# Performance work log

Measured on AMD Instinct MI355X. Metric: run time of the kernel, lower is better.

Reference implementation:

```python
import jax, jax.numpy as jnp
import numpy as np

B, LC, LQ, D = 16, 2048, 1024, 512


def setup_inputs() -> dict:
    key = jax.random.key(0)
    k1, k2, k3 = jax.random.split(key, 3)
    context = jax.random.normal(k1, (B, LC, D), dtype=jnp.float32)
    query = jax.random.normal(k2, (LQ, D), dtype=jnp.float32)
    # nn.Linear(3*D, 1, bias=False).weight  -> [1, 3D]
    w = jax.random.normal(k3, (1, 3 * D), dtype=jnp.float32) * (1.0 / np.sqrt(3 * D))
    return {"context": context, "query": query, "w": w}


def reference(context, query, w):
    # context: [B, Lc, D], query: [Lq, D], w: [1, 3D]
    d = context.shape[-1]
    wc, wq, wm = w[0, :d], w[0, d:2 * d], w[0, 2 * d:]
    # S[b,i,j] = <context[b,i], wc> + <query[j], wq> + <context[b,i]*wm, query[j]>
    # (algebraic collapse of Linear(cat(c, q, c*q)) -- identical math, no 4D tensor)
    S = ((context @ wc)[:, :, None]
         + (query @ wq)[None, None, :]
         + jnp.einsum('bid,jd->bij', context * wm, query))  # [B, Lc, Lq]
    # softmax over context dim (dim=1), then permute -> A[b,j,i]
    A = jnp.transpose(jax.nn.softmax(S, axis=1), (0, 2, 1))  # [B, Lq, Lc]
    # query mask: sign(|sum_d query|), same for every batch element
    qmask = jnp.sign(jnp.abs(jnp.sum(query, axis=-1)))  # [Lq]
    A = A * qmask[None, :, None]
    # attd[b,j,i,d] = A[b,j,i] * context[b,i,d]
    # G_att[b,i,d] = context[b,i,d] * sum_j A[b,j,i]
    colsum = jnp.sum(A, axis=1)  # [B, Lc]
    G_att = context * colsum[:, :, None]  # [B, Lc, D]
    # H[b,j,d] = sum_i A[b,j,i] * context[b,i,d]
    H = jnp.einsum('bji,bid->bjd', A, context)  # [B, Lq, D]
    G = jnp.concatenate((context, G_att), axis=2)  # [B, Lc, 2D]
    return (G, H)
```

## Files before the change

kernel.cpp:

```cpp
#include <hip/hip_runtime.h>
#include <stdint.h>

#define BB 16
#define LC 2048
#define LQ 1024
#define DD 512

typedef _Float16 f16x8 __attribute__((ext_vector_type(8)));
typedef _Float16 f16x4 __attribute__((ext_vector_type(4)));
typedef float f32x4 __attribute__((ext_vector_type(4)));

#define MFMA16 __builtin_amdgcn_mfma_f32_16x16x32_f16

__device__ __forceinline__ void async16(_Float16* lds, const _Float16* g) {
    __builtin_amdgcn_global_load_lds(
        (const __attribute__((address_space(1))) void*)g,
        (__attribute__((address_space(3))) void*)lds, 16, 0, 0);
}

__global__ void zero_k(float* __restrict__ p, int n) {
    int i = blockIdx.x * blockDim.x + threadIdx.x;
    if (i < n) p[i] = 0.0f;
}

__global__ __launch_bounds__(256) void prep_ctx(
    const float* __restrict__ ctx, const float* __restrict__ w,
    _Float16* __restrict__ cm, _Float16* __restrict__ ct, float* __restrict__ cb)
{
    __shared__ _Float16 sm[64][68];
    const int b = blockIdx.z;
    const int i0 = blockIdx.y * 64;
    const int d0 = blockIdx.x * 64;
    const int t = threadIdx.x;
    const int tx = t & 15, ty = t >> 4;
    const float* wc = w;
    const float* wm = w + 2 * DD;
    const float4 wc4 = *(const float4*)(wc + d0 + tx * 4);
    const float4 wm4 = *(const float4*)(wm + d0 + tx * 4);
    for (int k = 0; k < 4; ++k) {
        const int r = ty + 16 * k;
        const int ig = i0 + r;
        const float4 v = *(const float4*)(ctx + ((size_t)(b * LC + ig)) * DD + d0 + tx * 4);
        f16x4 cmv = { (_Float16)(v.x * wm4.x), (_Float16)(v.y * wm4.y),
                      (_Float16)(v.z * wm4.z), (_Float16)(v.w * wm4.w) };
        *(f16x4*)(cm + ((size_t)(b * LC + ig)) * DD + d0 + tx * 4) = cmv;
        sm[tx * 4 + 0][r] = (_Float16)v.x;
        sm[tx * 4 + 1][r] = (_Float16)v.y;
        sm[tx * 4 + 2][r] = (_Float16)v.z;
        sm[tx * 4 + 3][r] = (_Float16)v.w;
        float p = v.x * wc4.x + v.y * wc4.y + v.z * wc4.z + v.w * wc4.w;
        p += __shfl_xor(p, 1); p += __shfl_xor(p, 2);
        p += __shfl_xor(p, 4); p += __shfl_xor(p, 8);
        if (tx == 0) atomicAdd(&cb[b * LC + ig], p);
    }
    __syncthreads();
    for (int k = 0; k < 4; ++k) {
        const int dd = ty + 16 * k;
        f16x4 o = *(const f16x4*)(&sm[dd][tx * 4]);
        *(f16x4*)(ct + ((size_t)(b * DD + d0 + dd)) * LC + i0 + tx * 4) = o;
    }
}

__global__ __launch_bounds__(128) void prep_q(
    const float* __restrict__ q, const float* __restrict__ w,
    _Float16* __restrict__ qh, float* __restrict__ qb, float* __restrict__ qmask)
{
    const int j = blockIdx.x;
    const int t = threadIdx.x;
    const float* wq = w + DD;
    const float4 v = *(const float4*)(q + (size_t)j * DD + t * 4);
    const float4 wq4 = *(const float4*)(wq + t * 4);
    f16x4 qv = { (_Float16)v.x, (_Float16)v.y, (_Float16)v.z, (_Float16)v.w };
    *(f16x4*)(qh + (size_t)j * DD + t * 4) = qv;
    float dq = v.x * wq4.x + v.y * wq4.y + v.z * wq4.z + v.w * wq4.w;
    float sq = v.x + v.y + v.z + v.w;
    for (int m = 1; m < 64; m <<= 1) { dq += __shfl_xor(dq, m); sq += __shfl_xor(sq, m); }
    __shared__ float sd[2], ss[2];
    if ((t & 63) == 0) { sd[t >> 6] = dq; ss[t >> 6] = sq; }
    __syncthreads();
    if (t == 0) {
        qb[j] = sd[0] + sd[1];
        float s = ss[0] + ss[1];
        qmask[j] = (s != 0.0f) ? 1.0f : 0.0f;
    }
}

__global__ __launch_bounds__(256) void gemm1(
    const _Float16* __restrict__ qh, const _Float16* __restrict__ cm,
    const float* __restrict__ cb, const float* __restrict__ qb,
    _Float16* __restrict__ E, float* __restrict__ lsum)
{
    __shared__ __align__(16) _Float16 smA[128 * 32];
    __shared__ __align__(16) _Float16 smB[128 * 32];
    const int b = blockIdx.z;
    const int m0 = blockIdx.x * 128;
    const int n0 = blockIdx.y * 128;
    const int t = threadIdx.x;
    const int lane = t & 63;
    const int wid = t >> 6;
    const int wvm = wid >> 1, wvn = wid & 1;
    const int li = lane & 15, lg = lane >> 4;
    f32x4 acc[4][4] = {};
    const int srow = lane >> 2;
    const int scol = (lane & 3) * 8;
    const _Float16* gA0 = qh + (size_t)(m0 + wid * 32 + srow) * DD + scol;
    const _Float16* gA1 = gA0 + (size_t)16 * DD;
    const _Float16* gB0 = cm + ((size_t)(b * LC + n0 + wid * 32 + srow)) * DD + scol;
    const _Float16* gB1 = gB0 + (size_t)16 * DD;
    _Float16* sA0 = smA + wid * 32 * 32;
    _Float16* sA1 = sA0 + 16 * 32;
    _Float16* sB0 = smB + wid * 32 * 32;
    _Float16* sB1 = sB0 + 16 * 32;
    for (int ks = 0; ks < DD; ks += 32) {
        __syncthreads();
        async16(sA0, gA0 + ks);
        async16(sA1, gA1 + ks);
        async16(sB0, gB0 + ks);
        async16(sB1, gB1 + ks);
        __syncthreads();
        f16x8 af[4], bf[4];
        #pragma unroll
        for (int mt = 0; mt < 4; ++mt)
            af[mt] = *(const f16x8*)(smA + (wvm * 64 + mt * 16 + li) * 32 + lg * 8);
        #pragma unroll
        for (int nt = 0; nt < 4; ++nt)
            bf[nt] = *(const f16x8*)(smB + (wvn * 64 + nt * 16 + li) * 32 + lg * 8);
        #pragma unroll
        for (int mt = 0; mt < 4; ++mt)
            #pragma unroll
            for (int nt = 0; nt < 4; ++nt)
                acc[mt][nt] = MFMA16(af[mt], bf[nt], acc[mt][nt], 0, 0, 0);
    }
    __syncthreads();
    float* rs = (float*)smA;
    if (t < 128) rs[t] = 0.0f;
    __syncthreads();
    float cbv[4];
    #pragma unroll
    for (int nt = 0; nt < 4; ++nt) cbv[nt] = cb[b * LC + n0 + wvn * 64 + nt * 16 + li];
    #pragma unroll
    for (int mt = 0; mt < 4; ++mt) {
        #pragma unroll
        for (int r = 0; r < 4; ++r) {
            const int jl = wvm * 64 + mt * 16 + lg * 4 + r;
            const int j = m0 + jl;
            const float qbv = qb[j];
            _Float16* Erow = E + ((size_t)(b * LQ + j)) * LC + n0 + wvn * 64;
            float rsv = 0.0f;
            #pragma unroll
            for (int nt = 0; nt < 4; ++nt) {
                float e = __expf(acc[mt][nt][r] + cbv[nt] + qbv);
                rsv += e;
                Erow[nt * 16 + li] = (_Float16)e;
            }
            rsv += __shfl_xor(rsv, 1); rsv += __shfl_xor(rsv, 2);
            rsv += __shfl_xor(rsv, 4); rsv += __shfl_xor(rsv, 8);
            if (li == 0) atomicAdd(&rs[jl], rsv);
        }
    }
    __syncthreads();
    if (t < 128) atomicAdd(&lsum[b * LQ + m0 + t], rs[t]);
}

__global__ __launch_bounds__(256) void gemm2(
    const _Float16* __restrict__ E, const _Float16* __restrict__ ct,
    const float* __restrict__ lsum, const float* __restrict__ qmask,
    float* __restrict__ H)
{
    __shared__ __align__(16) _Float16 smA[128 * 32];
    __shared__ __align__(16) _Float16 smB[128 * 32];
    const int b = blockIdx.z;
    const int m0 = blockIdx.x * 128;
    const int n0 = blockIdx.y * 128;
    const int t = threadIdx.x;
    const int lane = t & 63;
    const int wid = t >> 6;
    const int wvm = wid >> 1, wvn = wid & 1;
    const int li = lane & 15, lg = lane >> 4;
    f32x4 acc[4][4] = {};
    const int srow = lane >> 2;
    const int scol = (lane & 3) * 8;
    const _Float16* gA0 = E + ((size_t)(b * LQ + m0 + wid * 32 + srow)) * LC + scol;
    const _Float16* gA1 = gA0 + (size_t)16 * LC;
    const _Float16* gB0 = ct + ((size_t)(b * DD + n0 + wid * 32 + srow)) * LC + scol;
    const _Float16* gB1 = gB0 + (size_t)16 * LC;
    _Float16* sA0 = smA + wid * 32 * 32;
    _Float16* sA1 = sA0 + 16 * 32;
    _Float16* sB0 = smB + wid * 32 * 32;
    _Float16* sB1 = sB0 + 16 * 32;
    for (int ks = 0; ks < LC; ks += 32) {
        __syncthreads();
        async16(sA0, gA0 + ks);
        async16(sA1, gA1 + ks);
        async16(sB0, gB0 + ks);
        async16(sB1, gB1 + ks);
        __syncthreads();
        f16x8 af[4], bf[4];
        #pragma unroll
        for (int mt = 0; mt < 4; ++mt)
            af[mt] = *(const f16x8*)(smA + (wvm * 64 + mt * 16 + li) * 32 + lg * 8);
        #pragma unroll
        for (int nt = 0; nt < 4; ++nt)
            bf[nt] = *(const f16x8*)(smB + (wvn * 64 + nt * 16 + li) * 32 + lg * 8);
        #pragma unroll
        for (int mt = 0; mt < 4; ++mt)
            #pragma unroll
            for (int nt = 0; nt < 4; ++nt)
                acc[mt][nt] = MFMA16(af[mt], bf[nt], acc[mt][nt], 0, 0, 0);
    }
    #pragma unroll
    for (int mt = 0; mt < 4; ++mt) {
        #pragma unroll
        for (int r = 0; r < 4; ++r) {
            const int j = m0 + wvm * 64 + mt * 16 + lg * 4 + r;
            const float s = qmask[j] / lsum[b * LQ + j];
            float* Hrow = H + ((size_t)(b * LQ + j)) * DD + n0 + wvn * 64;
            #pragma unroll
            for (int nt = 0; nt < 4; ++nt)
                Hrow[nt * 16 + li] = acc[mt][nt][r] * s;
        }
    }
}

__global__ __launch_bounds__(256) void colsum_k(
    const _Float16* __restrict__ E, const float* __restrict__ lsum,
    const float* __restrict__ qmask, float* __restrict__ cs)
{
    __shared__ float ssm[64];
    const int b = blockIdx.y;
    const int j0 = blockIdx.x * 64;
    const int t = threadIdx.x;
    if (t < 64) {
        const int jj = j0 + t;
        ssm[t] = qmask[jj] / lsum[b * LQ + jj];
    }
    __syncthreads();
    const _Float16* Eb = E + ((size_t)(b * LQ + j0)) * LC + t * 8;
    float acc[8] = {};
    #pragma unroll 4
    for (int j = 0; j < 64; ++j) {
        f16x8 v = *(const f16x8*)(Eb + (size_t)j * LC);
        const float s = ssm[j];
        #pragma unroll
        for (int q = 0; q < 8; ++q) acc[q] += s * (float)v[q];
    }
    float* base = cs + b * LC + t * 8;
    #pragma unroll
    for (int q = 0; q < 8; ++q) atomicAdd(base + q, acc[q]);
}

__global__ __launch_bounds__(128) void gwrite(
    const float* __restrict__ ctx, const float* __restrict__ cs, float* __restrict__ G)
{
    const int b = blockIdx.y, i = blockIdx.x, t = threadIdx.x;
    const float c = cs[b * LC + i];
    const size_t ro = (size_t)(b * LC + i);
    const float4 v = *(const float4*)(ctx + ro * DD + t * 4);
    float4 u; u.x = v.x * c; u.y = v.y * c; u.z = v.z * c; u.w = v.w * c;
    *(float4*)(G + ro * (2 * DD) + t * 4) = v;
    *(float4*)(G + ro * (2 * DD) + DD + t * 4) = u;
}

extern "C" void kernel_launch(void* const* d_in, const int* in_sizes, int n_in,
                              void* d_out, int out_size, void* d_ws, size_t ws_size,
                              hipStream_t stream)
{
    (void)in_sizes; (void)n_in; (void)out_size; (void)ws_size;
    const float* ctx = (const float*)d_in[0];
    const float* qry = (const float*)d_in[1];
    const float* w   = (const float*)d_in[2];
    float* G = (float*)d_out;
    float* H = G + (size_t)BB * LC * (2 * DD);

    char* ws = (char*)d_ws;
    _Float16* E  = (_Float16*)ws;
    _Float16* cm = (_Float16*)(ws + ((size_t)64 << 20));
    _Float16* ct = (_Float16*)(ws + ((size_t)96 << 20));
    _Float16* qh = (_Float16*)(ws + ((size_t)128 << 20));
    float* stats = (float*)(ws + ((size_t)130 << 20));
    float* cb    = stats;
    float* lsum  = cb + BB * LC;
    float* cs    = lsum + BB * LQ;
    float* qb    = cs + BB * LC;
    float* qmask = qb + LQ;

    const int nzero = BB * LC + BB * LQ + BB * LC;
    zero_k<<<dim3((nzero + 255) / 256), 256, 0, stream>>>(stats, nzero);
    prep_ctx<<<dim3(DD / 64, LC / 64, BB), 256, 0, stream>>>(ctx, w, cm, ct, cb);
    prep_q<<<dim3(LQ), 128, 0, stream>>>(qry, w, qh, qb, qmask);
    gemm1<<<dim3(LQ / 128, LC / 128, BB), 256, 0, stream>>>(qh, cm, cb, qb, E, lsum);
    gemm2<<<dim3(LQ / 128, DD / 128, BB), 256, 0, stream>>>(E, ct, lsum, qmask, H);
    colsum_k<<<dim3(LQ / 64, BB), 256, 0, stream>>>(E, lsum, qmask, cs);
    gwrite<<<dim3(LC, BB), 128, 0, stream>>>(ctx, cs, G);
}
```

Measured before the change: 390.9 us.

## Swap GEMM operand roles for vectorized epilogues, remap blocks, drop qb, atomic-free colsum

```diff
diff --git a/kernel.cpp b/kernel.cpp
--- a/kernel.cpp
+++ b/kernel.cpp
@@ -62,39 +62,33 @@
 }
 
 __global__ __launch_bounds__(128) void prep_q(
-    const float* __restrict__ q, const float* __restrict__ w,
-    _Float16* __restrict__ qh, float* __restrict__ qb, float* __restrict__ qmask)
+    const float* __restrict__ q, _Float16* __restrict__ qh, float* __restrict__ qmask)
 {
     const int j = blockIdx.x;
     const int t = threadIdx.x;
-    const float* wq = w + DD;
     const float4 v = *(const float4*)(q + (size_t)j * DD + t * 4);
-    const float4 wq4 = *(const float4*)(wq + t * 4);
     f16x4 qv = { (_Float16)v.x, (_Float16)v.y, (_Float16)v.z, (_Float16)v.w };
     *(f16x4*)(qh + (size_t)j * DD + t * 4) = qv;
-    float dq = v.x * wq4.x + v.y * wq4.y + v.z * wq4.z + v.w * wq4.w;
     float sq = v.x + v.y + v.z + v.w;
-    for (int m = 1; m < 64; m <<= 1) { dq += __shfl_xor(dq, m); sq += __shfl_xor(sq, m); }
-    __shared__ float sd[2], ss[2];
-    if ((t & 63) == 0) { sd[t >> 6] = dq; ss[t >> 6] = sq; }
-    __syncthreads();
-    if (t == 0) {
-        qb[j] = sd[0] + sd[1];
-        float s = ss[0] + ss[1];
-        qmask[j] = (s != 0.0f) ? 1.0f : 0.0f;
-    }
+    for (int m = 1; m < 64; m <<= 1) sq += __shfl_xor(sq, m);
+    __shared__ float ss[2];
+    if ((t & 63) == 0) ss[t >> 6] = sq;
+    __syncthreads();
+    if (t == 0) qmask[j] = ((ss[0] + ss[1]) != 0.0f) ? 1.0f : 0.0f;
 }
 
 __global__ __launch_bounds__(256) void gemm1(
     const _Float16* __restrict__ qh, const _Float16* __restrict__ cm,
-    const float* __restrict__ cb, const float* __restrict__ qb,
+    const float* __restrict__ cb,
     _Float16* __restrict__ E, float* __restrict__ lsum)
 {
     __shared__ __align__(16) _Float16 smA[128 * 32];
     __shared__ __align__(16) _Float16 smB[128 * 32];
-    const int b = blockIdx.z;
-    const int m0 = blockIdx.x * 128;
-    const int n0 = blockIdx.y * 128;
+    int orig = blockIdx.x + 16 * (blockIdx.y + 8 * blockIdx.z);
+    int wg = (orig & 7) * (2048 >> 3) + (orig >> 3);
+    const int m0 = (wg & 15) * 128;
+    const int n0 = ((wg >> 4) & 7) * 128;
+    const int b  = wg >> 7;
     const int t = threadIdx.x;
     const int lane = t & 63;
     const int wid = t >> 6;
@@ -103,9 +97,9 @@
     f32x4 acc[4][4] = {};
     const int srow = lane >> 2;
     const int scol = (lane & 3) * 8;
-    const _Float16* gA0 = qh + (size_t)(m0 + wid * 32 + srow) * DD + scol;
+    const _Float16* gA0 = cm + ((size_t)(b * LC + m0 + wid * 32 + srow)) * DD + scol;
     const _Float16* gA1 = gA0 + (size_t)16 * DD;
-    const _Float16* gB0 = cm + ((size_t)(b * LC + n0 + wid * 32 + srow)) * DD + scol;
+    const _Float16* gB0 = qh + (size_t)(n0 + wid * 32 + srow) * DD + scol;
     const _Float16* gB1 = gB0 + (size_t)16 * DD;
     _Float16* sA0 = smA + wid * 32 * 32;
     _Float16* sA1 = sA0 + 16 * 32;
@@ -135,31 +129,33 @@
     float* rs = (float*)smA;
     if (t < 128) rs[t] = 0.0f;
     __syncthreads();
-    float cbv[4];
-    #pragma unroll
-    for (int nt = 0; nt < 4; ++nt) cbv[nt] = cb[b * LC + n0 + wvn * 64 + nt * 16 + li];
-    #pragma unroll
-    for (int mt = 0; mt < 4; ++mt) {
-        #pragma unroll
-        for (int r = 0; r < 4; ++r) {
-            const int jl = wvm * 64 + mt * 16 + lg * 4 + r;
-            const int j = m0 + jl;
-            const float qbv = qb[j];
-            _Float16* Erow = E + ((size_t)(b * LQ + j)) * LC + n0 + wvn * 64;
-            float rsv = 0.0f;
+    f32x4 cb4[4];
+    #pragma unroll
+    for (int mt = 0; mt < 4; ++mt)
+        cb4[mt] = *(const f32x4*)(cb + b * LC + m0 + wvm * 64 + mt * 16 + lg * 4);
+    #pragma unroll
+    for (int nt = 0; nt < 4; ++nt) {
+        const int jl = wvn * 64 + nt * 16 + li;
+        const int j = n0 + jl;
+        _Float16* Ej = E + ((size_t)(b * LQ + j)) * LC + m0 + wvm * 64;
+        float rsv = 0.0f;
+        #pragma unroll
+        for (int mt = 0; mt < 4; ++mt) {
+            f16x4 ev;
             #pragma unroll
-            for (int nt = 0; nt < 4; ++nt) {
-                float e = __expf(acc[mt][nt][r] + cbv[nt] + qbv);
+            for (int r = 0; r < 4; ++r) {
+                float e = __expf(acc[mt][nt][r] + cb4[mt][r]);
                 rsv += e;
-                Erow[nt * 16 + li] = (_Float16)e;
+                ev[r] = (_Float16)e;
             }
-            rsv += __shfl_xor(rsv, 1); rsv += __shfl_xor(rsv, 2);
-            rsv += __shfl_xor(rsv, 4); rsv += __shfl_xor(rsv, 8);
-            if (li == 0) atomicAdd(&rs[jl], rsv);
+            *(f16x4*)(Ej + mt * 16 + lg * 4) = ev;
         }
-    }
-    __syncthreads();
-    if (t < 128) atomicAdd(&lsum[b * LQ + m0 + t], rs[t]);
+        rsv += __shfl_xor(rsv, 16);
+        rsv += __shfl_xor(rsv, 32);
+        if (lg == 0) atomicAdd(&rs[jl], rsv);
+    }
+    __syncthreads();
+    if (t < 128) atomicAdd(&lsum[b * LQ + n0 + t], rs[t]);
 }
 
 __global__ __launch_bounds__(256) void gemm2(
@@ -169,9 +165,11 @@
 {
     __shared__ __align__(16) _Float16 smA[128 * 32];
     __shared__ __align__(16) _Float16 smB[128 * 32];
-    const int b = blockIdx.z;
-    const int m0 = blockIdx.x * 128;
-    const int n0 = blockIdx.y * 128;
+    int orig = blockIdx.x + 4 * (blockIdx.y + 8 * blockIdx.z);
+    int wg = (orig & 7) * (512 >> 3) + (orig >> 3);
+    const int m0 = (wg & 3) * 128;
+    const int n0 = ((wg >> 2) & 7) * 128;
+    const int b  = wg >> 5;
     const int t = threadIdx.x;
     const int lane = t & 63;
     const int wid = t >> 6;
@@ -180,9 +178,9 @@
     f32x4 acc[4][4] = {};
     const int srow = lane >> 2;
     const int scol = (lane & 3) * 8;
-    const _Float16* gA0 = E + ((size_t)(b * LQ + m0 + wid * 32 + srow)) * LC + scol;
+    const _Float16* gA0 = ct + ((size_t)(b * DD + m0 + wid * 32 + srow)) * LC + scol;
     const _Float16* gA1 = gA0 + (size_t)16 * LC;
-    const _Float16* gB0 = ct + ((size_t)(b * DD + n0 + wid * 32 + srow)) * LC + scol;
+    const _Float16* gB0 = E + ((size_t)(b * LQ + n0 + wid * 32 + srow)) * LC + scol;
     const _Float16* gB1 = gB0 + (size_t)16 * LC;
     _Float16* sA0 = smA + wid * 32 * 32;
     _Float16* sA1 = sA0 + 16 * 32;
@@ -209,15 +207,14 @@
                 acc[mt][nt] = MFMA16(af[mt], bf[nt], acc[mt][nt], 0, 0, 0);
     }
     #pragma unroll
-    for (int mt = 0; mt < 4; ++mt) {
-        #pragma unroll
-        for (int r = 0; r < 4; ++r) {
-            const int j = m0 + wvm * 64 + mt * 16 + lg * 4 + r;
-            const float s = qmask[j] / lsum[b * LQ + j];
-            float* Hrow = H + ((size_t)(b * LQ + j)) * DD + n0 + wvn * 64;
-            #pragma unroll
-            for (int nt = 0; nt < 4; ++nt)
-                Hrow[nt * 16 + li] = acc[mt][nt][r] * s;
+    for (int nt = 0; nt < 4; ++nt) {
+        const int j = n0 + wvn * 64 + nt * 16 + li;
+        const float s = qmask[j] / lsum[b * LQ + j];
+        float* Hj = H + ((size_t)(b * LQ + j)) * DD + m0 + wvm * 64;
+        #pragma unroll
+        for (int mt = 0; mt < 4; ++mt) {
+            f32x4 o = acc[mt][nt] * s;
+            *(f32x4*)(Hj + mt * 16 + lg * 4) = o;
         }
     }
 }
@@ -226,27 +223,33 @@
     const _Float16* __restrict__ E, const float* __restrict__ lsum,
     const float* __restrict__ qmask, float* __restrict__ cs)
 {
-    __shared__ float ssm[64];
+    __shared__ float sscale[LQ];
+    __shared__ float red[16][132];
     const int b = blockIdx.y;
-    const int j0 = blockIdx.x * 64;
-    const int t = threadIdx.x;
-    if (t < 64) {
-        const int jj = j0 + t;
-        ssm[t] = qmask[jj] / lsum[b * LQ + jj];
-    }
-    __syncthreads();
-    const _Float16* Eb = E + ((size_t)(b * LQ + j0)) * LC + t * 8;
+    const int i0 = blockIdx.x * 128;
+    const int t = threadIdx.x;
+    for (int j = t; j < LQ; j += 256) sscale[j] = qmask[j] / lsum[b * LQ + j];
+    __syncthreads();
+    const int iw = t & 15;
+    const int jg = t >> 4;
+    const _Float16* Eb = E + ((size_t)(b * LQ + jg * 64)) * LC + i0 + iw * 8;
     float acc[8] = {};
     #pragma unroll 4
-    for (int j = 0; j < 64; ++j) {
-        f16x8 v = *(const f16x8*)(Eb + (size_t)j * LC);
-        const float s = ssm[j];
+    for (int k = 0; k < 64; ++k) {
+        f16x8 v = *(const f16x8*)(Eb + (size_t)k * LC);
+        const float s = sscale[jg * 64 + k];
         #pragma unroll
         for (int q = 0; q < 8; ++q) acc[q] += s * (float)v[q];
     }
-    float* base = cs + b * LC + t * 8;
-    #pragma unroll
-    for (int q = 0; q < 8; ++q) atomicAdd(base + q, acc[q]);
+    #pragma unroll
+    for (int q = 0; q < 8; ++q) red[jg][iw * 8 + q] = acc[q];
+    __syncthreads();
+    if (t < 128) {
+        float s = 0.0f;
+        #pragma unroll
+        for (int g = 0; g < 16; ++g) s += red[g][t];
+        cs[b * LC + i0 + t] = s;
+    }
 }
 
 __global__ __launch_bounds__(128) void gwrite(
@@ -281,15 +284,14 @@
     float* cb    = stats;
     float* lsum  = cb + BB * LC;
     float* cs    = lsum + BB * LQ;
-    float* qb    = cs + BB * LC;
-    float* qmask = qb + LQ;
-
-    const int nzero = BB * LC + BB * LQ + BB * LC;
+    float* qmask = cs + BB * LC;
+
+    const int nzero = BB * LC + BB * LQ;
     zero_k<<<dim3((nzero + 255) / 256), 256, 0, stream>>>(stats, nzero);
     prep_ctx<<<dim3(DD / 64, LC / 64, BB), 256, 0, stream>>>(ctx, w, cm, ct, cb);
-    prep_q<<<dim3(LQ), 128, 0, stream>>>(qry, w, qh, qb, qmask);
-    gemm1<<<dim3(LQ / 128, LC / 128, BB), 256, 0, stream>>>(qh, cm, cb, qb, E, lsum);
-    gemm2<<<dim3(LQ / 128, DD / 128, BB), 256, 0, stream>>>(E, ct, lsum, qmask, H);
-    colsum_k<<<dim3(LQ / 64, BB), 256, 0, stream>>>(E, lsum, qmask, cs);
+    prep_q<<<dim3(LQ), 128, 0, stream>>>(qry, qh, qmask);
+    gemm1<<<dim3(LC / 128, LQ / 128, BB), 256, 0, stream>>>(qh, cm, cb, E, lsum);
+    gemm2<<<dim3(DD / 128, LQ / 128, BB), 256, 0, stream>>>(E, ct, lsum, qmask, H);
+    colsum_k<<<dim3(LC / 128, BB), 256, 0, stream>>>(E, lsum, qmask, cs);
     gwrite<<<dim3(LC, BB), 128, 0, stream>>>(ctx, cs, G);
 }
```

Measured after the change: 357.5 us. 1.09x faster.
